# Kernel optimization log

Hardware: AMD Instinct MI355X
Metric: run time of the kernel (lower is better)

## Reference

```python
import jax, jax.numpy as jnp
import numpy as np

K = 32
D = 64
N_ITER = 10


def setup_inputs() -> dict:
    key = jax.random.key(0)
    k1, k2 = jax.random.split(key)
    B = 65536
    x = jax.random.normal(k1, (B, D), dtype=jnp.float32)
    c = jnp.zeros((K,), dtype=jnp.float32)
    mu = jax.random.normal(k2, (K, D), dtype=jnp.float32) * 0.1
    A = jnp.tile(jnp.eye(D, dtype=jnp.float32)[None], (K, 1, 1))
    alpha = jnp.float32(0.1)
    return {"x": x, "c": c, "mu": mu, "A": A, "alpha": alpha}


def _grad_phi(x, c, mu, A):
    # Precision matrices Sigma_i^{-1} = A_i^T A_i : (k, d, d)
    P = jnp.einsum('kji,kjl->kil', A, A)
    diff = x[:, None, :] - mu[None, :, :]          # (B, k, d)
    Pd = jnp.einsum('kij,bkj->bki', P, diff)       # Sigma^{-1} (x - mu)
    quad = jnp.einsum('bki,bki->bk', diff, Pd)     # (B, k)
    # Analytic gradient of phi(x) = logsumexp_i(c_i - 0.5 q_i):
    # grad = -sum_i softmax_i(c_i - 0.5 q_i) * Sigma_i^{-1}(x - mu_i)
    w = jax.nn.softmax(c[None, :] - 0.5 * quad, axis=1)  # (B, k)
    return -jnp.einsum('bk,bki->bi', w, Pd)


def reference(x, c, mu, A, alpha):
    def step(x_cur, _):
        x_new = x_cur + alpha * _grad_phi(x_cur, c, mu, A)
        return x_new, None
    x_final, _ = jax.lax.scan(step, x, None, length=N_ITER)
    return x_final
```

## Files before the change

### kernel.cpp

```cpp
#include <hip/hip_runtime.h>
#include <hip/hip_bf16.h>


typedef __attribute__((ext_vector_type(4))) float f32x4;
typedef __attribute__((ext_vector_type(8))) short bf16x8;

#define KC 32
#define NITER 10
#define XROW 72
#define WT_PITCH 40
#define PW_BYTES 7168

static __device__ __forceinline__ unsigned pk_bf16(float a, float b) {
  __hip_bfloat16 ha = __float2bfloat16(a), hb = __float2bfloat16(b);
  unsigned short ua = *(unsigned short*)&ha, ub = *(unsigned short*)&hb;
  return (unsigned)ua | ((unsigned)ub << 16);
}

static __device__ __forceinline__ float red16(float x) {
#if __has_builtin(__builtin_amdgcn_permlane16_swap)
  int xi = __float_as_int(x);
  auto pr = __builtin_amdgcn_permlane16_swap(xi, xi, false, false);
  return __int_as_float(pr[0]) + __int_as_float(pr[1]);
#else
  int v = __builtin_amdgcn_ds_swizzle(__float_as_int(x), 0x401F);
  return x + __int_as_float(v);
#endif
}
static __device__ __forceinline__ float red32(float x) {
  int xi = __float_as_int(x);
  auto pr = __builtin_amdgcn_permlane32_swap(xi, xi, false, false);
  return __int_as_float(pr[0]) + __int_as_float(pr[1]);
}

__global__ void precompute1(const float* __restrict__ A, const float* __restrict__ mu,
                            const float* __restrict__ c,
                            float* __restrict__ Pmu_g, float* __restrict__ e_g,
                            __hip_bfloat16* __restrict__ Psw) {
  __shared__ float As[64 * 64];
  __shared__ float Pk[64 * 64];
  const int k = blockIdx.x, tid = threadIdx.x;
  const float* Ak = A + k * 4096;
  for (int idx = tid; idx < 1024; idx += 256)
    *(f32x4*)&As[idx * 4] = *(const f32x4*)&Ak[idx * 4];
  __syncthreads();

  const int i = tid >> 2, lg = tid & 3;
  float acc[16] = {};
  for (int j = 0; j < 64; ++j) {
    float ai = As[j * 64 + i];
    const f32x4* row = (const f32x4*)&As[j * 64 + lg * 16];
#pragma unroll
    for (int g = 0; g < 4; ++g) {
      f32x4 v = row[g];
#pragma unroll
      for (int r = 0; r < 4; ++r) acc[g * 4 + r] += ai * v[r];
    }
  }
#pragma unroll
  for (int g = 0; g < 4; ++g)
#pragma unroll
    for (int r = 0; r < 4; ++r) Pk[i * 64 + lg * 16 + g * 4 + r] = acc[g * 4 + r];
  __syncthreads();

  if (tid < 64) {
    float s = 0.f;
    for (int l = 0; l < 64; ++l) s += Pk[l * 64 + tid] * mu[k * 64 + l];
    Pmu_g[k * 64 + tid] = s;
    float v = mu[k * 64 + tid] * s;
#pragma unroll
    for (int off = 1; off < 64; off <<= 1) v += __shfl_xor(v, off, 64);
    if (tid == 0) e_g[k] = c[k] - 0.5f * v;
  }

  unsigned* Psw32 = (unsigned*)(Psw + k * 4096);
  for (int idx2 = tid; idx2 < 2048; idx2 += 256) {
    int idx = idx2 << 1;
    int f = idx >> 9, ln = (idx >> 3) & 63, j = idx & 7;
    int mt = f >> 1, s = f & 1, qq = ln >> 4, l4 = ln & 15;
    int col = mt * 16 + l4, rb = s * 32 + qq * 8 + j;
    Psw32[idx2] = pk_bf16(Pk[rb * 64 + col], Pk[(rb + 1) * 64 + col]);
  }
}

__global__ void precompute2(const float* __restrict__ Pmu_g,
                            __hip_bfloat16* __restrict__ PmuA,
                            __hip_bfloat16* __restrict__ PmuB) {
  const int tid = threadIdx.x;
  for (int idx = tid; idx < 2048; idx += 256) {
    int f = idx >> 9, lane = (idx >> 3) & 63, j = idx & 7;
    int mtc = f >> 1, s = f & 1, qq = lane >> 4, l4 = lane & 15;
    PmuA[idx] = __float2bfloat16(Pmu_g[(mtc * 16 + l4) * 64 + s * 32 + qq * 8 + j]);
  }
  for (int idx = tid; idx < 2048; idx += 256) {
    int f = idx >> 9, lane = (idx >> 3) & 63, j = idx & 7;
    int qq = lane >> 4, l4 = lane & 15;
    PmuB[idx] = __float2bfloat16(Pmu_g[(qq * 8 + j) * 64 + f * 16 + l4]);
  }
}

__launch_bounds__(256, 2)
__global__ void denoise_main(const float* __restrict__ x_in,
                             const float* __restrict__ e_g,
                             const float* __restrict__ alpha_g,
                             const __hip_bfloat16* __restrict__ Psw,
                             const __hip_bfloat16* __restrict__ PmuA,
                             const __hip_bfloat16* __restrict__ PmuB,
                             float* __restrict__ out) {
  __shared__ __attribute__((aligned(16))) char scratch[4 * PW_BYTES];

  const int tid = threadIdx.x;
  const int wave = tid >> 6, lane = tid & 63;
  const int q = lane >> 4, l4 = lane & 15;
  const int base_pt = blockIdx.x * 128 + wave * 32;
  const float alpha = alpha_g[0];

  char* pw = scratch + wave * PW_BYTES;
  __hip_bfloat16* xsw = (__hip_bfloat16*)pw;
  float* pmxw = (float*)pw;
  __hip_bfloat16* wtw = (__hip_bfloat16*)(pw + 4608);

  const bf16x8* PswF = (const bf16x8*)Psw;
  const bf16x8* PmuAF = (const bf16x8*)PmuA;
  const bf16x8* PmuBF = (const bf16x8*)PmuB;

  f32x4 xm[4][2];
#pragma unroll
  for (int mt = 0; mt < 4; ++mt)
#pragma unroll
    for (int nt = 0; nt < 2; ++nt)
      xm[mt][nt] = *(const f32x4*)&x_in[(base_pt + nt * 16 + l4) * 64 + mt * 16 + q * 4];

  f32x4 ev[2];
#pragma unroll
  for (int mtc = 0; mtc < 2; ++mtc) ev[mtc] = *(const f32x4*)&e_g[mtc * 16 + q * 4];

  const f32x4 Z4 = {0.f, 0.f, 0.f, 0.f};

#pragma unroll 1
  for (int it = 0; it < NITER; ++it) {
#pragma unroll
    for (int mt = 0; mt < 4; ++mt)
#pragma unroll
      for (int nt = 0; nt < 2; ++nt) {
        uint2 v;
        v.x = pk_bf16(xm[mt][nt][0], xm[mt][nt][1]);
        v.y = pk_bf16(xm[mt][nt][2], xm[mt][nt][3]);
        *(uint2*)&xsw[(nt * 16 + l4) * XROW + mt * 16 + q * 4] = v;
      }

    bf16x8 bx[2][2];
#pragma unroll
    for (int s = 0; s < 2; ++s)
#pragma unroll
      for (int nt = 0; nt < 2; ++nt)
        bx[s][nt] = *(const bf16x8*)&xsw[(nt * 16 + l4) * XROW + s * 32 + q * 8];

    bf16x8 ap[2][4][2];
#pragma unroll
    for (int mt = 0; mt < 4; ++mt)
#pragma unroll
      for (int s = 0; s < 2; ++s)
        ap[0][mt][s] = PswF[(mt * 2 + s) * 64 + lane];

    f32x4 pmx[2][2];
#pragma unroll
    for (int mtc = 0; mtc < 2; ++mtc)
#pragma unroll
      for (int nt = 0; nt < 2; ++nt)
        pmx[mtc][nt] =
            __builtin_amdgcn_mfma_f32_16x16x32_bf16(PmuAF[(mtc * 2) * 64 + lane], bx[0][nt], Z4, 0, 0, 0);
#pragma unroll
    for (int mtc = 0; mtc < 2; ++mtc)
#pragma unroll
      for (int nt = 0; nt < 2; ++nt)
        pmx[mtc][nt] = __builtin_amdgcn_mfma_f32_16x16x32_bf16(PmuAF[(mtc * 2 + 1) * 64 + lane],
                                                               bx[1][nt], pmx[mtc][nt], 0, 0, 0);
#pragma unroll
    for (int mtc = 0; mtc < 2; ++mtc)
#pragma unroll
      for (int nt = 0; nt < 2; ++nt)
#pragma unroll
        for (int r = 0; r < 4; ++r)
          pmxw[(mtc * 16 + q * 4 + r) * 32 + nt * 16 + l4] = pmx[mtc][nt][r] + ev[mtc][r];

    f32x4 accY[4][2];
#pragma unroll
    for (int mt = 0; mt < 4; ++mt)
#pragma unroll
      for (int nt = 0; nt < 2; ++nt) accY[mt][nt] = Z4;
    float lsum0 = 0.f, lsum1 = 0.f;

#pragma unroll 2
    for (int k = 0; k < KC; ++k) {
      const int cur = k & 1, nxt = cur ^ 1;
      const int kn = (k + 1) & (KC - 1);
#pragma unroll
      for (int mt = 0; mt < 4; ++mt)
#pragma unroll
        for (int s = 0; s < 2; ++s)
          ap[nxt][mt][s] = PswF[kn * 512 + (mt * 2 + s) * 64 + lane];

      f32x4 y[4][2];
#pragma unroll
      for (int mt = 0; mt < 4; ++mt)
#pragma unroll
        for (int nt = 0; nt < 2; ++nt)
          y[mt][nt] = __builtin_amdgcn_mfma_f32_16x16x32_bf16(ap[cur][mt][0], bx[0][nt], Z4, 0, 0, 0);
#pragma unroll
      for (int mt = 0; mt < 4; ++mt)
#pragma unroll
        for (int nt = 0; nt < 2; ++nt)
          y[mt][nt] =
              __builtin_amdgcn_mfma_f32_16x16x32_bf16(ap[cur][mt][1], bx[1][nt], y[mt][nt], 0, 0, 0);

      f32x4 d0 = xm[0][0] * y[0][0];
      f32x4 d1 = xm[0][1] * y[0][1];
#pragma unroll
      for (int mt = 1; mt < 4; ++mt) {
        d0 += xm[mt][0] * y[mt][0];
        d1 += xm[mt][1] * y[mt][1];
      }
      float xy0 = (d0[0] + d0[1]) + (d0[2] + d0[3]);
      float xy1 = (d1[0] + d1[1]) + (d1[2] + d1[3]);
      xy0 = red32(red16(xy0));
      xy1 = red32(red16(xy1));

      const float pk0 = pmxw[k * 32 + l4];
      const float pk1 = pmxw[k * 32 + 16 + l4];
      const float w0 = __expf(pk0 - 0.5f * xy0);
      const float w1 = __expf(pk1 - 0.5f * xy1);
      lsum0 += w0;
      lsum1 += w1;
      if (q == 0) {
        wtw[l4 * WT_PITCH + k] = __float2bfloat16(w0);
        wtw[(16 + l4) * WT_PITCH + k] = __float2bfloat16(w1);
      }
#pragma unroll
      for (int mt = 0; mt < 4; ++mt) {
        accY[mt][0] += w0 * y[mt][0];
        accY[mt][1] += w1 * y[mt][1];
      }
    }

    bf16x8 wtf[2];
#pragma unroll
    for (int nt = 0; nt < 2; ++nt)
      wtf[nt] = *(const bf16x8*)&wtw[(nt * 16 + l4) * WT_PITCH + q * 8];
    f32x4 pacc[4][2];
#pragma unroll
    for (int mt = 0; mt < 4; ++mt) {
      bf16x8 a = PmuBF[mt * 64 + lane];
      pacc[mt][0] = __builtin_amdgcn_mfma_f32_16x16x32_bf16(a, wtf[0], Z4, 0, 0, 0);
      pacc[mt][1] = __builtin_amdgcn_mfma_f32_16x16x32_bf16(a, wtf[1], Z4, 0, 0, 0);
    }

    const float c0 = alpha / lsum0;
    const float c1 = alpha / lsum1;
#pragma unroll
    for (int mt = 0; mt < 4; ++mt) {
      xm[mt][0] += c0 * (pacc[mt][0] - accY[mt][0]);
      xm[mt][1] += c1 * (pacc[mt][1] - accY[mt][1]);
    }
  }

#pragma unroll
  for (int mt = 0; mt < 4; ++mt)
#pragma unroll
    for (int nt = 0; nt < 2; ++nt)
      *(f32x4*)&out[(base_pt + nt * 16 + l4) * 64 + mt * 16 + q * 4] = xm[mt][nt];
}

extern "C" void kernel_launch(void* const* d_in, const int* in_sizes, int n_in,
                              void* d_out, int out_size, void* d_ws, size_t ws_size,
                              hipStream_t stream) {
  (void)in_sizes; (void)n_in; (void)out_size; (void)ws_size;
  const float* x = (const float*)d_in[0];
  const float* c = (const float*)d_in[1];
  const float* mu = (const float*)d_in[2];
  const float* A = (const float*)d_in[3];
  const float* alpha = (const float*)d_in[4];
  float* out = (float*)d_out;

  char* ws = (char*)d_ws;
  float* Pmu_g = (float*)(ws);
  float* e_g = (float*)(ws + 8192);
  __hip_bfloat16* PmuA = (__hip_bfloat16*)(ws + 8448);
  __hip_bfloat16* PmuB = (__hip_bfloat16*)(ws + 12544);
  __hip_bfloat16* Psw = (__hip_bfloat16*)(ws + 16640);

  precompute1<<<32, 256, 0, stream>>>(A, mu, c, Pmu_g, e_g, Psw);
  precompute2<<<1, 256, 0, stream>>>(Pmu_g, PmuA, PmuB);
  denoise_main<<<512, 256, 0, stream>>>(x, e_g, alpha, Psw, PmuA, PmuB, out);
}
```

Measured before the change: 283.9 us.

## Software-pipeline k-loop so MFMAs for next component overlap softmax chain

Result: slower. 551.0 us (+94.1%).

```diff
diff --git a/kernel.cpp b/kernel.cpp
--- a/kernel.cpp
+++ b/kernel.cpp
@@ -137,8 +137,64 @@
 
   const f32x4 Z4 = {0.f, 0.f, 0.f, 0.f};
 
+  bf16x8 apA[4][2], apB[4][2];
+  f32x4 yA[4][2], yB[4][2];
+  f32x4 accY[4][2];
+  float lsum0, lsum1;
+  bf16x8 bx[2][2];
+
+  auto loadap = [&](bf16x8(&ap)[4][2], int k) {
+#pragma unroll
+    for (int mt = 0; mt < 4; ++mt)
+#pragma unroll
+      for (int s = 0; s < 2; ++s) ap[mt][s] = PswF[k * 512 + (mt * 2 + s) * 64 + lane];
+  };
+  auto mfma16 = [&](f32x4(&y)[4][2], const bf16x8(&ap)[4][2]) {
+#pragma unroll
+    for (int mt = 0; mt < 4; ++mt)
+#pragma unroll
+      for (int nt = 0; nt < 2; ++nt)
+        y[mt][nt] = __builtin_amdgcn_mfma_f32_16x16x32_bf16(ap[mt][0], bx[0][nt], Z4, 0, 0, 0);
+#pragma unroll
+    for (int mt = 0; mt < 4; ++mt)
+#pragma unroll
+      for (int nt = 0; nt < 2; ++nt)
+        y[mt][nt] = __builtin_amdgcn_mfma_f32_16x16x32_bf16(ap[mt][1], bx[1][nt], y[mt][nt], 0, 0, 0);
+  };
+  auto chain = [&](const f32x4(&y)[4][2], int k) {
+    f32x4 d0 = xm[0][0] * y[0][0];
+    f32x4 d1 = xm[0][1] * y[0][1];
+#pragma unroll
+    for (int mt = 1; mt < 4; ++mt) {
+      d0 += xm[mt][0] * y[mt][0];
+      d1 += xm[mt][1] * y[mt][1];
+    }
+    float xy0 = (d0[0] + d0[1]) + (d0[2] + d0[3]);
+    float xy1 = (d1[0] + d1[1]) + (d1[2] + d1[3]);
+    xy0 = red32(red16(xy0));
+    xy1 = red32(red16(xy1));
+    const float pk0 = pmxw[k * 32 + l4];
+    const float pk1 = pmxw[k * 32 + 16 + l4];
+    const float w0 = __expf(pk0 - 0.5f * xy0);
+    const float w1 = __expf(pk1 - 0.5f * xy1);
+    lsum0 += w0;
+    lsum1 += w1;
+    if (q == 0) {
+      wtw[l4 * WT_PITCH + k] = __float2bfloat16(w0);
+      wtw[(16 + l4) * WT_PITCH + k] = __float2bfloat16(w1);
+    }
+#pragma unroll
+    for (int mt = 0; mt < 4; ++mt) {
+      accY[mt][0] += w0 * y[mt][0];
+      accY[mt][1] += w1 * y[mt][1];
+    }
+  };
+
 #pragma unroll 1
   for (int it = 0; it < NITER; ++it) {
+    loadap(apA, 0);
+    loadap(apB, 1);
+
 #pragma unroll
     for (int mt = 0; mt < 4; ++mt)
 #pragma unroll
@@ -149,19 +205,11 @@
         *(uint2*)&xsw[(nt * 16 + l4) * XROW + mt * 16 + q * 4] = v;
       }
 
-    bf16x8 bx[2][2];
 #pragma unroll
     for (int s = 0; s < 2; ++s)
 #pragma unroll
       for (int nt = 0; nt < 2; ++nt)
         bx[s][nt] = *(const bf16x8*)&xsw[(nt * 16 + l4) * XROW + s * 32 + q * 8];
-
-    bf16x8 ap[2][4][2];
-#pragma unroll
-    for (int mt = 0; mt < 4; ++mt)
-#pragma unroll
-      for (int s = 0; s < 2; ++s)
-        ap[0][mt][s] = PswF[(mt * 2 + s) * 64 + lane];
 
     f32x4 pmx[2][2];
 #pragma unroll
@@ -184,64 +232,28 @@
         for (int r = 0; r < 4; ++r)
           pmxw[(mtc * 16 + q * 4 + r) * 32 + nt * 16 + l4] = pmx[mtc][nt][r] + ev[mtc][r];
 
-    f32x4 accY[4][2];
 #pragma unroll
     for (int mt = 0; mt < 4; ++mt)
 #pragma unroll
       for (int nt = 0; nt < 2; ++nt) accY[mt][nt] = Z4;
-    float lsum0 = 0.f, lsum1 = 0.f;
-
-#pragma unroll 2
-    for (int k = 0; k < KC; ++k) {
-      const int cur = k & 1, nxt = cur ^ 1;
-      const int kn = (k + 1) & (KC - 1);
-#pragma unroll
-      for (int mt = 0; mt < 4; ++mt)
-#pragma unroll
-        for (int s = 0; s < 2; ++s)
-          ap[nxt][mt][s] = PswF[kn * 512 + (mt * 2 + s) * 64 + lane];
-
-      f32x4 y[4][2];
-#pragma unroll
-      for (int mt = 0; mt < 4; ++mt)
-#pragma unroll
-        for (int nt = 0; nt < 2; ++nt)
-          y[mt][nt] = __builtin_amdgcn_mfma_f32_16x16x32_bf16(ap[cur][mt][0], bx[0][nt], Z4, 0, 0, 0);
-#pragma unroll
-      for (int mt = 0; mt < 4; ++mt)
-#pragma unroll
-        for (int nt = 0; nt < 2; ++nt)
-          y[mt][nt] =
-              __builtin_amdgcn_mfma_f32_16x16x32_bf16(ap[cur][mt][1], bx[1][nt], y[mt][nt], 0, 0, 0);
-
-      f32x4 d0 = xm[0][0] * y[0][0];
-      f32x4 d1 = xm[0][1] * y[0][1];
-#pragma unroll
-      for (int mt = 1; mt < 4; ++mt) {
-        d0 += xm[mt][0] * y[mt][0];
-        d1 += xm[mt][1] * y[mt][1];
-      }
-      float xy0 = (d0[0] + d0[1]) + (d0[2] + d0[3]);
-      float xy1 = (d1[0] + d1[1]) + (d1[2] + d1[3]);
-      xy0 = red32(red16(xy0));
-      xy1 = red32(red16(xy1));
-
-      const float pk0 = pmxw[k * 32 + l4];
-      const float pk1 = pmxw[k * 32 + 16 + l4];
-      const float w0 = __expf(pk0 - 0.5f * xy0);
-      const float w1 = __expf(pk1 - 0.5f * xy1);
-      lsum0 += w0;
-      lsum1 += w1;
-      if (q == 0) {
-        wtw[l4 * WT_PITCH + k] = __float2bfloat16(w0);
-        wtw[(16 + l4) * WT_PITCH + k] = __float2bfloat16(w1);
-      }
-#pragma unroll
-      for (int mt = 0; mt < 4; ++mt) {
-        accY[mt][0] += w0 * y[mt][0];
-        accY[mt][1] += w1 * y[mt][1];
-      }
-    }
+    lsum0 = 0.f;
+    lsum1 = 0.f;
+
+    mfma16(yA, apA);
+    loadap(apA, 2);
+#pragma unroll 1
+    for (int kp = 0; kp < 15; ++kp) {
+      const int k0 = 2 * kp;
+      mfma16(yB, apB);
+      loadap(apB, k0 + 3);
+      chain(yA, k0);
+      mfma16(yA, apA);
+      loadap(apA, (k0 + 4) & 31);
+      chain(yB, k0 + 1);
+    }
+    mfma16(yB, apB);
+    chain(yA, 30);
+    chain(yB, 31);
 
     bf16x8 wtf[2];
 #pragma unroll
```

## Stage precision matrices into LDS via async global_load_lds ring buffer

Applied to the files above, without the earlier changes.

After: 292.8 us. 3.1% more time.

```diff
diff --git a/kernel.cpp b/kernel.cpp
--- a/kernel.cpp
+++ b/kernel.cpp
@@ -10,6 +10,8 @@
 #define XROW 72
 #define WT_PITCH 40
 #define PW_BYTES 7168
+#define PSTG 8192
+#define NBUF 4
 
 static __device__ __forceinline__ unsigned pk_bf16(float a, float b) {
   __hip_bfloat16 ha = __float2bfloat16(a), hb = __float2bfloat16(b);
@@ -31,6 +33,12 @@
   int xi = __float_as_int(x);
   auto pr = __builtin_amdgcn_permlane32_swap(xi, xi, false, false);
   return __int_as_float(pr[0]) + __int_as_float(pr[1]);
+}
+
+static __device__ __forceinline__ void stage16(const void* gsrc, void* ldst) {
+  __builtin_amdgcn_global_load_lds(
+      (const __attribute__((address_space(1))) unsigned int*)gsrc,
+      (__attribute__((address_space(3))) unsigned int*)ldst, 16, 0, 0);
 }
 
 __global__ void precompute1(const float* __restrict__ A, const float* __restrict__ mu,
@@ -107,7 +115,7 @@
                              const __hip_bfloat16* __restrict__ PmuA,
                              const __hip_bfloat16* __restrict__ PmuB,
                              float* __restrict__ out) {
-  __shared__ __attribute__((aligned(16))) char scratch[4 * PW_BYTES];
+  __shared__ __attribute__((aligned(16))) char scratch[4 * PW_BYTES + NBUF * PSTG];
 
   const int tid = threadIdx.x;
   const int wave = tid >> 6, lane = tid & 63;
@@ -119,8 +127,9 @@
   __hip_bfloat16* xsw = (__hip_bfloat16*)pw;
   float* pmxw = (float*)pw;
   __hip_bfloat16* wtw = (__hip_bfloat16*)(pw + 4608);
-
-  const bf16x8* PswF = (const bf16x8*)Psw;
+  char* pstg = scratch + 4 * PW_BYTES;
+
+  const char* PswB = (const char*)Psw;
   const bf16x8* PmuAF = (const bf16x8*)PmuA;
   const bf16x8* PmuBF = (const bf16x8*)PmuB;
 
@@ -136,6 +145,12 @@
   for (int mtc = 0; mtc < 2; ++mtc) ev[mtc] = *(const f32x4*)&e_g[mtc * 16 + q * 4];
 
   const f32x4 Z4 = {0.f, 0.f, 0.f, 0.f};
+  const int f0 = 2 * wave, f1 = 2 * wave + 1;
+
+  stage16(PswB + f0 * 1024 + lane * 16, pstg + f0 * 1024);
+  stage16(PswB + f1 * 1024 + lane * 16, pstg + f1 * 1024);
+  stage16(PswB + PSTG + f0 * 1024 + lane * 16, pstg + PSTG + f0 * 1024);
+  stage16(PswB + PSTG + f1 * 1024 + lane * 16, pstg + PSTG + f1 * 1024);
 
 #pragma unroll 1
   for (int it = 0; it < NITER; ++it) {
@@ -156,13 +171,6 @@
       for (int nt = 0; nt < 2; ++nt)
         bx[s][nt] = *(const bf16x8*)&xsw[(nt * 16 + l4) * XROW + s * 32 + q * 8];
 
-    bf16x8 ap[2][4][2];
-#pragma unroll
-    for (int mt = 0; mt < 4; ++mt)
-#pragma unroll
-      for (int s = 0; s < 2; ++s)
-        ap[0][mt][s] = PswF[(mt * 2 + s) * 64 + lane];
-
     f32x4 pmx[2][2];
 #pragma unroll
     for (int mtc = 0; mtc < 2; ++mtc)
@@ -191,28 +199,40 @@
       for (int nt = 0; nt < 2; ++nt) accY[mt][nt] = Z4;
     float lsum0 = 0.f, lsum1 = 0.f;
 
+    asm volatile("s_waitcnt vmcnt(2)" ::: "memory");
+    __builtin_amdgcn_s_barrier();
+    asm volatile("" ::: "memory");
+
 #pragma unroll 2
     for (int k = 0; k < KC; ++k) {
-      const int cur = k & 1, nxt = cur ^ 1;
-      const int kn = (k + 1) & (KC - 1);
+      {
+        const int ks = (k + 2) & (KC - 1);
+        const char* ps = PswB + ks * PSTG;
+        char* pd = pstg + (ks & (NBUF - 1)) * PSTG;
+        stage16(ps + f0 * 1024 + lane * 16, pd + f0 * 1024);
+        stage16(ps + f1 * 1024 + lane * 16, pd + f1 * 1024);
+      }
+
+      const char* pc = pstg + (k & (NBUF - 1)) * PSTG;
+      bf16x8 ap[4][2];
 #pragma unroll
       for (int mt = 0; mt < 4; ++mt)
 #pragma unroll
         for (int s = 0; s < 2; ++s)
-          ap[nxt][mt][s] = PswF[kn * 512 + (mt * 2 + s) * 64 + lane];
+          ap[mt][s] = *(const bf16x8*)(pc + (mt * 2 + s) * 1024 + lane * 16);
 
       f32x4 y[4][2];
 #pragma unroll
       for (int mt = 0; mt < 4; ++mt)
 #pragma unroll
         for (int nt = 0; nt < 2; ++nt)
-          y[mt][nt] = __builtin_amdgcn_mfma_f32_16x16x32_bf16(ap[cur][mt][0], bx[0][nt], Z4, 0, 0, 0);
+          y[mt][nt] = __builtin_amdgcn_mfma_f32_16x16x32_bf16(ap[mt][0], bx[0][nt], Z4, 0, 0, 0);
 #pragma unroll
       for (int mt = 0; mt < 4; ++mt)
 #pragma unroll
         for (int nt = 0; nt < 2; ++nt)
           y[mt][nt] =
-              __builtin_amdgcn_mfma_f32_16x16x32_bf16(ap[cur][mt][1], bx[1][nt], y[mt][nt], 0, 0, 0);
+              __builtin_amdgcn_mfma_f32_16x16x32_bf16(ap[mt][1], bx[1][nt], y[mt][nt], 0, 0, 0);
 
       f32x4 d0 = xm[0][0] * y[0][0];
       f32x4 d1 = xm[0][1] * y[0][1];
@@ -241,6 +261,10 @@
         accY[mt][0] += w0 * y[mt][0];
         accY[mt][1] += w1 * y[mt][1];
       }
+
+      asm volatile("s_waitcnt vmcnt(2)" ::: "memory");
+      __builtin_amdgcn_s_barrier();
+      asm volatile("" ::: "memory");
     }
 
     bf16x8 wtf[2];
```

## Fold Pmu bf16 swizzle into main kernel LDS and raise MFMA priority

Applied to the files above, without the earlier changes.

Measured after the change: 286.9 us. About the same (+1.1%).

```diff
diff --git a/kernel.cpp b/kernel.cpp
--- a/kernel.cpp
+++ b/kernel.cpp
@@ -83,31 +83,16 @@
   }
 }
 
-__global__ void precompute2(const float* __restrict__ Pmu_g,
-                            __hip_bfloat16* __restrict__ PmuA,
-                            __hip_bfloat16* __restrict__ PmuB) {
-  const int tid = threadIdx.x;
-  for (int idx = tid; idx < 2048; idx += 256) {
-    int f = idx >> 9, lane = (idx >> 3) & 63, j = idx & 7;
-    int mtc = f >> 1, s = f & 1, qq = lane >> 4, l4 = lane & 15;
-    PmuA[idx] = __float2bfloat16(Pmu_g[(mtc * 16 + l4) * 64 + s * 32 + qq * 8 + j]);
-  }
-  for (int idx = tid; idx < 2048; idx += 256) {
-    int f = idx >> 9, lane = (idx >> 3) & 63, j = idx & 7;
-    int qq = lane >> 4, l4 = lane & 15;
-    PmuB[idx] = __float2bfloat16(Pmu_g[(qq * 8 + j) * 64 + f * 16 + l4]);
-  }
-}
-
 __launch_bounds__(256, 2)
 __global__ void denoise_main(const float* __restrict__ x_in,
                              const float* __restrict__ e_g,
                              const float* __restrict__ alpha_g,
                              const __hip_bfloat16* __restrict__ Psw,
-                             const __hip_bfloat16* __restrict__ PmuA,
-                             const __hip_bfloat16* __restrict__ PmuB,
+                             const float* __restrict__ Pmu_g,
                              float* __restrict__ out) {
   __shared__ __attribute__((aligned(16))) char scratch[4 * PW_BYTES];
+  __shared__ __attribute__((aligned(16))) __hip_bfloat16 pmuA_s[2048];
+  __shared__ __attribute__((aligned(16))) __hip_bfloat16 pmuB_s[2048];
 
   const int tid = threadIdx.x;
   const int wave = tid >> 6, lane = tid & 63;
@@ -121,8 +106,17 @@
   __hip_bfloat16* wtw = (__hip_bfloat16*)(pw + 4608);
 
   const bf16x8* PswF = (const bf16x8*)Psw;
-  const bf16x8* PmuAF = (const bf16x8*)PmuA;
-  const bf16x8* PmuBF = (const bf16x8*)PmuB;
+
+  for (int idx = tid; idx < 2048; idx += 256) {
+    int f = idx >> 9, ln = (idx >> 3) & 63, j = idx & 7;
+    int mtc = f >> 1, s = f & 1, qq = ln >> 4, l4i = ln & 15;
+    pmuA_s[idx] = __float2bfloat16(Pmu_g[(mtc * 16 + l4i) * 64 + s * 32 + qq * 8 + j]);
+  }
+  for (int idx = tid; idx < 2048; idx += 256) {
+    int f = idx >> 9, ln = (idx >> 3) & 63, j = idx & 7;
+    int qq = ln >> 4, l4i = ln & 15;
+    pmuB_s[idx] = __float2bfloat16(Pmu_g[(qq * 8 + j) * 64 + f * 16 + l4i]);
+  }
 
   f32x4 xm[4][2];
 #pragma unroll
@@ -136,6 +130,10 @@
   for (int mtc = 0; mtc < 2; ++mtc) ev[mtc] = *(const f32x4*)&e_g[mtc * 16 + q * 4];
 
   const f32x4 Z4 = {0.f, 0.f, 0.f, 0.f};
+  const bf16x8* PmuAF = (const bf16x8*)pmuA_s;
+  const bf16x8* PmuBF = (const bf16x8*)pmuB_s;
+
+  __syncthreads();
 
 #pragma unroll 1
   for (int it = 0; it < NITER; ++it) {
@@ -164,6 +162,7 @@
         ap[0][mt][s] = PswF[(mt * 2 + s) * 64 + lane];
 
     f32x4 pmx[2][2];
+    __builtin_amdgcn_s_setprio(1);
 #pragma unroll
     for (int mtc = 0; mtc < 2; ++mtc)
 #pragma unroll
@@ -176,6 +175,7 @@
       for (int nt = 0; nt < 2; ++nt)
         pmx[mtc][nt] = __builtin_amdgcn_mfma_f32_16x16x32_bf16(PmuAF[(mtc * 2 + 1) * 64 + lane],
                                                                bx[1][nt], pmx[mtc][nt], 0, 0, 0);
+    __builtin_amdgcn_s_setprio(0);
 #pragma unroll
     for (int mtc = 0; mtc < 2; ++mtc)
 #pragma unroll
@@ -202,6 +202,7 @@
           ap[nxt][mt][s] = PswF[kn * 512 + (mt * 2 + s) * 64 + lane];
 
       f32x4 y[4][2];
+      __builtin_amdgcn_s_setprio(1);
 #pragma unroll
       for (int mt = 0; mt < 4; ++mt)
 #pragma unroll
@@ -213,6 +214,7 @@
         for (int nt = 0; nt < 2; ++nt)
           y[mt][nt] =
               __builtin_amdgcn_mfma_f32_16x16x32_bf16(ap[cur][mt][1], bx[1][nt], y[mt][nt], 0, 0, 0);
+      __builtin_amdgcn_s_setprio(0);
 
       f32x4 d0 = xm[0][0] * y[0][0];
       f32x4 d1 = xm[0][1] * y[0][1];
@@ -248,12 +250,14 @@
     for (int nt = 0; nt < 2; ++nt)
       wtf[nt] = *(const bf16x8*)&wtw[(nt * 16 + l4) * WT_PITCH + q * 8];
     f32x4 pacc[4][2];
+    __builtin_amdgcn_s_setprio(1);
 #pragma unroll
     for (int mt = 0; mt < 4; ++mt) {
       bf16x8 a = PmuBF[mt * 64 + lane];
       pacc[mt][0] = __builtin_amdgcn_mfma_f32_16x16x32_bf16(a, wtf[0], Z4, 0, 0, 0);
       pacc[mt][1] = __builtin_amdgcn_mfma_f32_16x16x32_bf16(a, wtf[1], Z4, 0, 0, 0);
     }
+    __builtin_amdgcn_s_setprio(0);
 
     const float c0 = alpha / lsum0;
     const float c1 = alpha / lsum1;
@@ -285,11 +289,8 @@
   char* ws = (char*)d_ws;
   float* Pmu_g = (float*)(ws);
   float* e_g = (float*)(ws + 8192);
-  __hip_bfloat16* PmuA = (__hip_bfloat16*)(ws + 8448);
-  __hip_bfloat16* PmuB = (__hip_bfloat16*)(ws + 12544);
   __hip_bfloat16* Psw = (__hip_bfloat16*)(ws + 16640);
 
   precompute1<<<32, 256, 0, stream>>>(A, mu, c, Pmu_g, e_g, Psw);
-  precompute2<<<1, 256, 0, stream>>>(Pmu_g, PmuA, PmuB);
-  denoise_main<<<512, 256, 0, stream>>>(x, e_g, alpha, Psw, PmuA, PmuB, out);
-}
+  denoise_main<<<512, 256, 0, stream>>>(x, e_g, alpha, Psw, Pmu_g, out);
+}
```
